# Performance work log

Measured on AMD Instinct MI355X. Metric: run time of the kernel, lower is better.

## Reference

```python
import jax, jax.numpy as jnp
import numpy as np

H, N, I, K = 1024, 16, 128, 2  # model dim, n_experts, expert inner dim (hardcoded in Expert), top-k
B, S = 4, 4096


def setup_inputs() -> dict:
    key = jax.random.key(0)
    ks = jax.random.split(key, 4)
    x = jax.random.normal(ks[0], (B, S, H), jnp.float32)
    Wr = jax.random.normal(ks[1], (N, H), jnp.float32) / np.sqrt(H)      # router Linear(h,n,bias=False) weight [n,h]
    Wg = jax.random.normal(ks[2], (N, I, H), jnp.float32) / np.sqrt(H)   # per-expert g: Linear(h,i) weight [i,h]
    bg = jnp.zeros((N, I), jnp.float32)
    Wu = jax.random.normal(ks[3], (N, H, I), jnp.float32) / np.sqrt(I)   # per-expert u: Linear(i,h) weight [h,i]
    bu = jnp.zeros((N, H), jnp.float32)
    return {"x": x, "Wr": Wr, "Wg": Wg, "bg": bg, "Wu": Wu, "bu": bu, "k": K}


def reference(x, Wr, Wg, bg, Wu, bu, k):
    b, s, h = x.shape
    n = Wr.shape[0]
    xf = x.reshape(-1, h)                      # [T, h]
    T = xf.shape[0]
    logits = xf @ Wr.T                          # [T, n]
    val, idx = jax.lax.top_k(logits, k)         # [T, k]
    w = jax.nn.softmax(val, axis=-1)            # softmax over selected top-k logits
    # scatter top-k weights into a dense [T, n] gate matrix (zero for unselected experts)
    gates = jnp.zeros((T, n), x.dtype).at[jnp.arange(T)[:, None], idx].set(w)
    # all-expert SwiGLU-free MLP: silu(x @ Wg^T + bg) @ Wu^T + bu, weighted combine by gates
    a = jax.nn.silu(jnp.einsum('th,nih->tni', xf, Wg) + bg)   # [T, n, i]
    out = jnp.einsum('tn,tni,nhi->th', gates, a, Wu) + gates @ bu
    return out.reshape(b, s, h)
```

## Files before the change

kernel.cpp:

```cpp
#include <hip/hip_runtime.h>
#include <hip/hip_fp16.h>

#define T_TOK 16384
#define HDIM  1024
#define NE    16
#define IDIM  128
#define BMq   64
#define NSLOT (T_TOK*2)
#define NSLOT_PAD (NSLOT + NE*BMq)
#define NBLK1 (NSLOT_PAD/BMq)

typedef _Float16 half8 __attribute__((ext_vector_type(8)));
typedef _Float16 half4 __attribute__((ext_vector_type(4)));
typedef float    f32x4 __attribute__((ext_vector_type(4)));

#define WS_TOKE 0
#define WS_TOKW 131072
#define WS_CNT  262144
#define WS_CUR  262208
#define WS_OFF  262272
#define WS_STOK 262400
#define WS_SW   397568
#define WS_ABUF 532736
#define WS_TSLOT 9183488ULL
#define WS_WG16  9314560ULL
#define WS_WU16  13508864ULL
#define WS_X16   17703168ULL
#define WS_OBUF  51257600ULL
#define WS_FULL_END 120463616ULL

template<bool WX>
__global__ __launch_bounds__(64) void router_k(const float* __restrict__ x,
                                               const float* __restrict__ Wr,
                                               int2* __restrict__ tok_e,
                                               float2* __restrict__ tok_w,
                                               _Float16* __restrict__ x16) {
    __shared__ __align__(16) _Float16 Ah[16*64], Al[16*64], Bh[16*64], Bl[16*64];
    int lane = threadIdx.x;
    int tile0 = blockIdx.x * 16;
    f32x4 accM = {0.f,0.f,0.f,0.f};
    f32x4 accC = {0.f,0.f,0.f,0.f};
    for (int kk = 0; kk < HDIM; kk += 64) {
        __syncthreads();
#pragma unroll
        for (int s = 0; s < 4; ++s) {
            int idx = lane + s*64;
            int r = idx >> 4, kq = idx & 15;
            float4 xv = *reinterpret_cast<const float4*>(x  + (size_t)(tile0 + r)*HDIM + kk + kq*4);
            float4 wv = *reinterpret_cast<const float4*>(Wr + (size_t)r*HDIM + kk + kq*4);
            half4 xh, xl, wh, wl;
            {
                float v0=xv.x,v1=xv.y,v2=xv.z,v3=xv.w;
                xh[0]=(_Float16)v0; xh[1]=(_Float16)v1; xh[2]=(_Float16)v2; xh[3]=(_Float16)v3;
                xl[0]=(_Float16)((v0-(float)xh[0])*2048.f); xl[1]=(_Float16)((v1-(float)xh[1])*2048.f);
                xl[2]=(_Float16)((v2-(float)xh[2])*2048.f); xl[3]=(_Float16)((v3-(float)xh[3])*2048.f);
                float w0=wv.x,w1=wv.y,w2=wv.z,w3=wv.w;
                wh[0]=(_Float16)w0; wh[1]=(_Float16)w1; wh[2]=(_Float16)w2; wh[3]=(_Float16)w3;
                wl[0]=(_Float16)((w0-(float)wh[0])*2048.f); wl[1]=(_Float16)((w1-(float)wh[1])*2048.f);
                wl[2]=(_Float16)((w2-(float)wh[2])*2048.f); wl[3]=(_Float16)((w3-(float)wh[3])*2048.f);
            }
            int sw = (kq*4) ^ ((r & 7) << 3);
            *reinterpret_cast<half4*>(&Ah[r*64 + sw]) = xh;
            *reinterpret_cast<half4*>(&Al[r*64 + sw]) = xl;
            *reinterpret_cast<half4*>(&Bh[r*64 + sw]) = wh;
            *reinterpret_cast<half4*>(&Bl[r*64 + sw]) = wl;
            if (WX)
                *reinterpret_cast<half4*>(x16 + (size_t)(tile0 + r)*HDIM + kk + kq*4) = xh;
        }
        __syncthreads();
        int rr = lane & 15;
        int swr = (rr & 7) << 3;
#pragma unroll
        for (int ks = 0; ks < 64; ks += 32) {
            int c = ks + ((lane >> 4) << 3);
            half8 axh = *reinterpret_cast<const half8*>(&Ah[rr*64 + (c ^ swr)]);
            half8 axl = *reinterpret_cast<const half8*>(&Al[rr*64 + (c ^ swr)]);
            half8 bwh = *reinterpret_cast<const half8*>(&Bh[rr*64 + (c ^ swr)]);
            half8 bwl = *reinterpret_cast<const half8*>(&Bl[rr*64 + (c ^ swr)]);
            accM = __builtin_amdgcn_mfma_f32_16x16x32_f16(axh, bwh, accM, 0, 0, 0);
            accC = __builtin_amdgcn_mfma_f32_16x16x32_f16(axh, bwl, accC, 0, 0, 0);
            accC = __builtin_amdgcn_mfma_f32_16x16x32_f16(axl, bwh, accC, 0, 0, 0);
        }
    }
    int c = lane & 15, g = lane >> 4;
#pragma unroll
    for (int j = 0; j < 4; ++j) {
        float v1 = accM[j] + accC[j] * (1.f/2048.f);
        int   i1 = c;
        float v2 = -1e30f; int i2 = 16;
#pragma unroll
        for (int m = 1; m < 16; m <<= 1) {
            float ov1 = __shfl_xor(v1, m); int oi1 = __shfl_xor(i1, m);
            float ov2 = __shfl_xor(v2, m); int oi2 = __shfl_xor(i2, m);
            float nv1, nv2; int ni1, ni2;
            bool aFirst = (v1 > ov1) || (v1 == ov1 && i1 < oi1);
            if (aFirst) {
                nv1 = v1; ni1 = i1;
                if ((v2 > ov1) || (v2 == ov1 && i2 < oi1)) { nv2 = v2; ni2 = i2; }
                else                                        { nv2 = ov1; ni2 = oi1; }
            } else {
                nv1 = ov1; ni1 = oi1;
                if ((ov2 > v1) || (ov2 == v1 && oi2 < i1)) { nv2 = ov2; ni2 = oi2; }
                else                                        { nv2 = v1; ni2 = i1; }
            }
            v1 = nv1; i1 = ni1; v2 = nv2; i2 = ni2;
        }
        if (c == 0) {
            int t = tile0 + g*4 + j;
            float e2 = __expf(v2 - v1);
            float inv = 1.f / (1.f + e2);
            tok_e[t] = make_int2(i1, i2);
            tok_w[t] = make_float2(inv, e2 * inv);
        }
    }
}

__global__ __launch_bounds__(256) void cvtw_k(const float* __restrict__ Wg,
                                              const float* __restrict__ Wu,
                                              _Float16* __restrict__ Wg16,
                                              _Float16* __restrict__ Wu16) {
    int i = blockIdx.x * 256 + threadIdx.x;
    float4 g = reinterpret_cast<const float4*>(Wg)[i];
    float4 u = reinterpret_cast<const float4*>(Wu)[i];
    half4 gh = {(_Float16)g.x,(_Float16)g.y,(_Float16)g.z,(_Float16)g.w};
    half4 uh = {(_Float16)u.x,(_Float16)u.y,(_Float16)u.z,(_Float16)u.w};
    reinterpret_cast<half4*>(Wg16)[i] = gh;
    reinterpret_cast<half4*>(Wu16)[i] = uh;
}

__global__ __launch_bounds__(256) void count_k(const int2* __restrict__ tok_e,
                                               int* __restrict__ counts) {
    int e = blockIdx.x;
    int c = 0;
    for (int t = threadIdx.x; t < T_TOK; t += 256) {
        int2 te = tok_e[t];
        c += (te.x == e) + (te.y == e);
    }
    __shared__ int red[256];
    red[threadIdx.x] = c; __syncthreads();
    for (int s = 128; s > 0; s >>= 1) {
        if (threadIdx.x < s) red[threadIdx.x] += red[threadIdx.x + s];
        __syncthreads();
    }
    if (threadIdx.x == 0) counts[e] = red[0];
}

__global__ void scan_k(const int* __restrict__ counts, int* __restrict__ offs) {
    if (threadIdx.x == 0) {
        int acc = 0;
        for (int e = 0; e < NE; ++e) {
            offs[e] = acc;
            acc += ((counts[e] + BMq - 1) / BMq) * BMq;
        }
        offs[NE] = acc;
    }
}

template<bool FULL>
__global__ __launch_bounds__(256) void scatter_k(const int2* __restrict__ tok_e,
                                                 const float2* __restrict__ tok_w,
                                                 const int* __restrict__ offs,
                                                 int* __restrict__ cursors,
                                                 int* __restrict__ slot_tok,
                                                 float* __restrict__ slot_w,
                                                 int2* __restrict__ tok_slots) {
    __shared__ int lcnt[NE];
    __shared__ int lbase[NE];
    if (threadIdx.x < NE) lcnt[threadIdx.x] = 0;
    __syncthreads();
    int t = blockIdx.x * 256 + threadIdx.x;
    int2 te = tok_e[t]; float2 tw = tok_w[t];
    int p0 = atomicAdd(&lcnt[te.x], 1);
    int p1 = atomicAdd(&lcnt[te.y], 1);
    __syncthreads();
    if (threadIdx.x < NE)
        lbase[threadIdx.x] = atomicAdd(&cursors[threadIdx.x], lcnt[threadIdx.x]);
    __syncthreads();
    int s0 = offs[te.x] + lbase[te.x] + p0;
    int s1 = offs[te.y] + lbase[te.y] + p1;
    slot_tok[s0] = t; slot_w[s0] = tw.x;
    slot_tok[s1] = t; slot_w[s1] = tw.y;
    if (FULL) tok_slots[t] = make_int2(s0, s1);
}

template<bool FULL>
__global__ __launch_bounds__(256) void gemm1_k(const float* __restrict__ x,
                                               const _Float16* __restrict__ x16,
                                               const float* __restrict__ Wg,
                                               const _Float16* __restrict__ Wg16,
                                               const float* __restrict__ bg,
                                               const int* __restrict__ offs,
                                               const int* __restrict__ slot_tok,
                                               _Float16* __restrict__ abuf) {
    __shared__ __align__(16) _Float16 As[64 * 64];
    __shared__ __align__(16) _Float16 Bs[128 * 64];
    __shared__ int tokLds[64];
    int row0 = blockIdx.x * BMq;
    if (row0 >= offs[NE]) return;
    int e = 0;
#pragma unroll
    for (int q = 1; q < NE; ++q) if (offs[q] <= row0) e = q;
    int tid = threadIdx.x;
    if (tid < 64) tokLds[tid] = slot_tok[row0 + tid];
    __syncthreads();
    int wv = tid >> 6, lane = tid & 63;
    f32x4 acc[4][2] = {};
    for (int kk = 0; kk < HDIM; kk += 64) {
        if (FULL) {
#pragma unroll
            for (int j = 0; j < 2; ++j) {
                int idx = tid + j * 256;
                int r = idx >> 3, hq = idx & 7;
                int tok = tokLds[r];
                half8 v = {0,0,0,0,0,0,0,0};
                if (tok >= 0) v = *reinterpret_cast<const half8*>(x16 + (size_t)tok * HDIM + kk + hq * 8);
                *reinterpret_cast<half8*>(&As[r * 64 + ((hq * 8) ^ ((r & 7) << 3))]) = v;
            }
#pragma unroll
            for (int j = 0; j < 4; ++j) {
                int idx = tid + j * 256;
                int r = idx >> 3, hq = idx & 7;
                half8 v = *reinterpret_cast<const half8*>(Wg16 + (size_t)e * IDIM * HDIM + (size_t)r * HDIM + kk + hq * 8);
                *reinterpret_cast<half8*>(&Bs[r * 64 + ((hq * 8) ^ ((r & 7) << 3))]) = v;
            }
        } else {
#pragma unroll
            for (int j = 0; j < 4; ++j) {
                int idx = tid + j * 256;
                int r = idx >> 4, kq = idx & 15;
                int tok = tokLds[r];
                float4 v = make_float4(0.f, 0.f, 0.f, 0.f);
                if (tok >= 0) v = *reinterpret_cast<const float4*>(x + (size_t)tok * HDIM + kk + kq * 4);
                half4 hv = {(_Float16)v.x, (_Float16)v.y, (_Float16)v.z, (_Float16)v.w};
                *reinterpret_cast<half4*>(&As[r * 64 + ((kq * 4) ^ ((r & 7) << 3))]) = hv;
            }
#pragma unroll 4
            for (int j = 0; j < 8; ++j) {
                int idx = tid + j * 256;
                int r = idx >> 4, kq = idx & 15;
                float4 v = *reinterpret_cast<const float4*>(Wg + (size_t)e * IDIM * HDIM + (size_t)r * HDIM + kk + kq * 4);
                half4 hv = {(_Float16)v.x, (_Float16)v.y, (_Float16)v.z, (_Float16)v.w};
                *reinterpret_cast<half4*>(&Bs[r * 64 + ((kq * 4) ^ ((r & 7) << 3))]) = hv;
            }
        }
        __syncthreads();
#pragma unroll
        for (int ks = 0; ks < 64; ks += 32) {
            int c = ks + ((lane >> 4) << 3);
            half8 af[4], bf[2];
#pragma unroll
            for (int rt = 0; rt < 4; ++rt) {
                int r = rt * 16 + (lane & 15);
                af[rt] = *reinterpret_cast<const half8*>(&As[r * 64 + (c ^ ((r & 7) << 3))]);
            }
#pragma unroll
            for (int ct = 0; ct < 2; ++ct) {
                int r = wv * 32 + ct * 16 + (lane & 15);
                bf[ct] = *reinterpret_cast<const half8*>(&Bs[r * 64 + (c ^ ((r & 7) << 3))]);
            }
#pragma unroll
            for (int rt = 0; rt < 4; ++rt)
#pragma unroll
                for (int ct = 0; ct < 2; ++ct)
                    acc[rt][ct] = __builtin_amdgcn_mfma_f32_16x16x32_f16(af[rt], bf[ct], acc[rt][ct], 0, 0, 0);
        }
        __syncthreads();
    }
#pragma unroll
    for (int rt = 0; rt < 4; ++rt)
#pragma unroll
        for (int ct = 0; ct < 2; ++ct) {
            int i = wv * 32 + ct * 16 + (lane & 15);
            float bgv = bg[e * IDIM + i];
#pragma unroll
            for (int j = 0; j < 4; ++j) {
                int m = rt * 16 + ((lane >> 4) << 2) + j;
                if (tokLds[m] >= 0) {
                    float v = acc[rt][ct][j] + bgv;
                    float sv = v / (1.f + __expf(-v));
                    abuf[(size_t)(row0 + m) * IDIM + i] = (_Float16)sv;
                }
            }
        }
}

template<bool FULL>
__global__ __launch_bounds__(256) void gemm2_k(const _Float16* __restrict__ abuf,
                                               const float* __restrict__ Wu,
                                               const _Float16* __restrict__ Wu16,
                                               const float* __restrict__ bu,
                                               const int* __restrict__ offs,
                                               const int* __restrict__ slot_tok,
                                               const float* __restrict__ slot_w,
                                               float* __restrict__ out,
                                               _Float16* __restrict__ Obuf) {
    __shared__ __align__(16) _Float16 As[64 * 128];
    __shared__ __align__(16) _Float16 Bs[128 * 128];
    __shared__ int   tokLds[64];
    __shared__ float wLds[64];
    int row0 = blockIdx.x * BMq;
    if (row0 >= offs[NE]) return;
    int h0 = blockIdx.y * 128;
    int e = 0;
#pragma unroll
    for (int q = 1; q < NE; ++q) if (offs[q] <= row0) e = q;
    int tid = threadIdx.x;
    if (tid < 64) { tokLds[tid] = slot_tok[row0 + tid]; wLds[tid] = slot_w[row0 + tid]; }
#pragma unroll
    for (int j = 0; j < 4; ++j) {
        int idx = tid + j * 256;
        int r = idx >> 4, hq = idx & 15;
        half8 v = *reinterpret_cast<const half8*>(abuf + (size_t)(row0 + r) * IDIM + hq * 8);
        *reinterpret_cast<half8*>(&As[r * 128 + ((hq * 8) ^ ((r & 7) << 3))]) = v;
    }
    if (FULL) {
#pragma unroll
        for (int j = 0; j < 8; ++j) {
            int idx = tid + j * 256;
            int r = idx >> 4, fq = idx & 15;
            half8 v = *reinterpret_cast<const half8*>(Wu16 + (size_t)e * HDIM * IDIM + (size_t)(h0 + r) * IDIM + fq * 8);
            *reinterpret_cast<half8*>(&Bs[r * 128 + ((fq * 8) ^ ((r & 7) << 3))]) = v;
        }
    } else {
#pragma unroll 4
        for (int j = 0; j < 16; ++j) {
            int idx = tid + j * 256;
            int r = idx >> 5, fq = idx & 31;
            float4 v = *reinterpret_cast<const float4*>(Wu + (size_t)e * HDIM * IDIM + (size_t)(h0 + r) * IDIM + fq * 4);
            half4 hv = {(_Float16)v.x, (_Float16)v.y, (_Float16)v.z, (_Float16)v.w};
            *reinterpret_cast<half4*>(&Bs[r * 128 + ((fq * 4) ^ ((r & 7) << 3))]) = hv;
        }
    }
    __syncthreads();
    int wv = tid >> 6, lane = tid & 63;
    f32x4 acc[4][2] = {};
#pragma unroll
    for (int ks = 0; ks < 128; ks += 32) {
        int c = ks + ((lane >> 4) << 3);
        half8 af[4], bf[2];
#pragma unroll
        for (int rt = 0; rt < 4; ++rt) {
            int r = rt * 16 + (lane & 15);
            af[rt] = *reinterpret_cast<const half8*>(&As[r * 128 + (c ^ ((r & 7) << 3))]);
        }
#pragma unroll
        for (int ct = 0; ct < 2; ++ct) {
            int r = wv * 32 + ct * 16 + (lane & 15);
            bf[ct] = *reinterpret_cast<const half8*>(&Bs[r * 128 + (c ^ ((r & 7) << 3))]);
        }
#pragma unroll
        for (int rt = 0; rt < 4; ++rt)
#pragma unroll
            for (int ct = 0; ct < 2; ++ct)
                acc[rt][ct] = __builtin_amdgcn_mfma_f32_16x16x32_f16(af[rt], bf[ct], acc[rt][ct], 0, 0, 0);
    }
#pragma unroll
    for (int rt = 0; rt < 4; ++rt)
#pragma unroll
        for (int ct = 0; ct < 2; ++ct) {
            int h = h0 + wv * 32 + ct * 16 + (lane & 15);
#pragma unroll
            for (int j = 0; j < 4; ++j) {
                int m = rt * 16 + ((lane >> 4) << 2) + j;
                if (FULL) {
                    Obuf[(size_t)(row0 + m) * HDIM + h] = (_Float16)acc[rt][ct][j];
                } else {
                    int tok = tokLds[m];
                    if (tok >= 0)
                        atomicAdd(out + (size_t)tok * HDIM + h,
                                  (acc[rt][ct][j] + bu[e * HDIM + h]) * wLds[m]);
                }
            }
        }
}

__global__ __launch_bounds__(256) void combine_k(const _Float16* __restrict__ Obuf,
                                                 const float* __restrict__ bu,
                                                 const int2* __restrict__ tok_slots,
                                                 const int2* __restrict__ tok_e,
                                                 const float2* __restrict__ tok_w,
                                                 float* __restrict__ out) {
    int wv = threadIdx.x >> 6, lane = threadIdx.x & 63;
    int t = blockIdx.x * 4 + wv;
    int2   sl = tok_slots[t];
    int2   te = tok_e[t];
    float2 tw = tok_w[t];
    const _Float16* O1 = Obuf + (size_t)sl.x * HDIM;
    const _Float16* O2 = Obuf + (size_t)sl.y * HDIM;
    const float* b1 = bu + (size_t)te.x * HDIM;
    const float* b2 = bu + (size_t)te.y * HDIM;
    float* op = out + (size_t)t * HDIM;
#pragma unroll
    for (int q = 0; q < 4; ++q) {
        int h = q * 256 + lane * 4;
        half4  a1 = *reinterpret_cast<const half4*>(O1 + h);
        half4  a2 = *reinterpret_cast<const half4*>(O2 + h);
        float4 v1 = *reinterpret_cast<const float4*>(b1 + h);
        float4 v2 = *reinterpret_cast<const float4*>(b2 + h);
        float4 o;
        o.x = tw.x * ((float)a1[0] + v1.x) + tw.y * ((float)a2[0] + v2.x);
        o.y = tw.x * ((float)a1[1] + v1.y) + tw.y * ((float)a2[1] + v2.y);
        o.z = tw.x * ((float)a1[2] + v1.z) + tw.y * ((float)a2[2] + v2.z);
        o.w = tw.x * ((float)a1[3] + v1.w) + tw.y * ((float)a2[3] + v2.w);
        *reinterpret_cast<float4*>(op + h) = o;
    }
}

extern "C" void kernel_launch(void* const* d_in, const int* in_sizes, int n_in,
                              void* d_out, int out_size, void* d_ws, size_t ws_size,
                              hipStream_t stream) {
    const float* x  = (const float*)d_in[0];
    const float* Wr = (const float*)d_in[1];
    const float* Wg = (const float*)d_in[2];
    const float* bg = (const float*)d_in[3];
    const float* Wu = (const float*)d_in[4];
    const float* bu = (const float*)d_in[5];
    float* out = (float*)d_out;
    char* ws = (char*)d_ws;

    int2*      tok_e    = (int2*)(ws + WS_TOKE);
    float2*    tok_w    = (float2*)(ws + WS_TOKW);
    int*       counts   = (int*)(ws + WS_CNT);
    int*       cursors  = (int*)(ws + WS_CUR);
    int*       offs     = (int*)(ws + WS_OFF);
    int*       slot_tok = (int*)(ws + WS_STOK);
    float*     slot_w   = (float*)(ws + WS_SW);
    _Float16*  abuf     = (_Float16*)(ws + WS_ABUF);
    int2*      tok_slots= (int2*)(ws + WS_TSLOT);
    _Float16*  Wg16     = (_Float16*)(ws + WS_WG16);
    _Float16*  Wu16     = (_Float16*)(ws + WS_WU16);
    _Float16*  x16      = (_Float16*)(ws + WS_X16);
    _Float16*  Obuf     = (_Float16*)(ws + WS_OBUF);

    const bool full = (ws_size >= WS_FULL_END);

    hipMemsetAsync(ws + WS_CNT, 0, 256, stream);
    hipMemsetAsync(slot_tok, 0xFF, NSLOT_PAD * sizeof(int), stream);

    if (full) {
        cvtw_k   <<<2048, 256, 0, stream>>>(Wg, Wu, Wg16, Wu16);
        router_k<true><<<T_TOK/16, 64, 0, stream>>>(x, Wr, tok_e, tok_w, x16);
        count_k  <<<NE, 256, 0, stream>>>(tok_e, counts);
        scan_k   <<<1, 64, 0, stream>>>(counts, offs);
        scatter_k<true><<<T_TOK/256, 256, 0, stream>>>(tok_e, tok_w, offs, cursors, slot_tok, slot_w, tok_slots);
        gemm1_k<true><<<NBLK1, 256, 0, stream>>>(x, x16, Wg, Wg16, bg, offs, slot_tok, abuf);
        dim3 g2(NBLK1, 8);
        gemm2_k<true><<<g2, 256, 0, stream>>>(abuf, Wu, Wu16, bu, offs, slot_tok, slot_w, out, Obuf);
        combine_k<<<T_TOK/4, 256, 0, stream>>>(Obuf, bu, tok_slots, tok_e, tok_w, out);
    } else {
        hipMemsetAsync(d_out, 0, (size_t)T_TOK * HDIM * sizeof(float), stream);
        router_k<false><<<T_TOK/16, 64, 0, stream>>>(x, Wr, tok_e, tok_w, nullptr);
        count_k  <<<NE, 256, 0, stream>>>(tok_e, counts);
        scan_k   <<<1, 64, 0, stream>>>(counts, offs);
        scatter_k<false><<<T_TOK/256, 256, 0, stream>>>(tok_e, tok_w, offs, cursors, slot_tok, slot_w, nullptr);
        gemm1_k<false><<<NBLK1, 256, 0, stream>>>(x, nullptr, Wg, nullptr, bg, offs, slot_tok, abuf);
        dim3 g2(NBLK1, 8);
        gemm2_k<false><<<g2, 256, 0, stream>>>(abuf, Wu, nullptr, bu, offs, slot_tok, slot_w, out, nullptr);
    }
}
```

Measured before the change: 285.3 us.

## Replace split-fp16 MFMA router with fp32 warp-per-token dot products

The router drops the hi/lo fp16 split MFMA GEMM with LDS staging and instead computes all 16 expert logits per token in fp32. Each wavefront handles one token at a time, with per-lane partial dot products and a butterfly shuffle reduction, then a serial top-2 in lane 0. This removes the LDS round trips, barriers and triple MFMA work, trading them for 16 full-wave shuffle reductions per token and repeated Wr loads that should mostly hit cache. The launch grid changes to 2048 blocks of 256 threads, each block covering 8 tokens.

New measurement: 274.8 us. -3.7%, faster.

```diff
diff --git a/kernel.cpp b/kernel.cpp
--- a/kernel.cpp
+++ b/kernel.cpp
@@ -30,83 +30,47 @@
 #define WS_FULL_END 120463616ULL
 
 template<bool WX>
-__global__ __launch_bounds__(64) void router_k(const float* __restrict__ x,
-                                               const float* __restrict__ Wr,
-                                               int2* __restrict__ tok_e,
-                                               float2* __restrict__ tok_w,
-                                               _Float16* __restrict__ x16) {
-    __shared__ __align__(16) _Float16 Ah[16*64], Al[16*64], Bh[16*64], Bl[16*64];
-    int lane = threadIdx.x;
-    int tile0 = blockIdx.x * 16;
-    f32x4 accM = {0.f,0.f,0.f,0.f};
-    f32x4 accC = {0.f,0.f,0.f,0.f};
-    for (int kk = 0; kk < HDIM; kk += 64) {
-        __syncthreads();
-#pragma unroll
-        for (int s = 0; s < 4; ++s) {
-            int idx = lane + s*64;
-            int r = idx >> 4, kq = idx & 15;
-            float4 xv = *reinterpret_cast<const float4*>(x  + (size_t)(tile0 + r)*HDIM + kk + kq*4);
-            float4 wv = *reinterpret_cast<const float4*>(Wr + (size_t)r*HDIM + kk + kq*4);
-            half4 xh, xl, wh, wl;
-            {
-                float v0=xv.x,v1=xv.y,v2=xv.z,v3=xv.w;
-                xh[0]=(_Float16)v0; xh[1]=(_Float16)v1; xh[2]=(_Float16)v2; xh[3]=(_Float16)v3;
-                xl[0]=(_Float16)((v0-(float)xh[0])*2048.f); xl[1]=(_Float16)((v1-(float)xh[1])*2048.f);
-                xl[2]=(_Float16)((v2-(float)xh[2])*2048.f); xl[3]=(_Float16)((v3-(float)xh[3])*2048.f);
-                float w0=wv.x,w1=wv.y,w2=wv.z,w3=wv.w;
-                wh[0]=(_Float16)w0; wh[1]=(_Float16)w1; wh[2]=(_Float16)w2; wh[3]=(_Float16)w3;
-                wl[0]=(_Float16)((w0-(float)wh[0])*2048.f); wl[1]=(_Float16)((w1-(float)wh[1])*2048.f);
-                wl[2]=(_Float16)((w2-(float)wh[2])*2048.f); wl[3]=(_Float16)((w3-(float)wh[3])*2048.f);
-            }
-            int sw = (kq*4) ^ ((r & 7) << 3);
-            *reinterpret_cast<half4*>(&Ah[r*64 + sw]) = xh;
-            *reinterpret_cast<half4*>(&Al[r*64 + sw]) = xl;
-            *reinterpret_cast<half4*>(&Bh[r*64 + sw]) = wh;
-            *reinterpret_cast<half4*>(&Bl[r*64 + sw]) = wl;
-            if (WX)
-                *reinterpret_cast<half4*>(x16 + (size_t)(tile0 + r)*HDIM + kk + kq*4) = xh;
-        }
-        __syncthreads();
-        int rr = lane & 15;
-        int swr = (rr & 7) << 3;
-#pragma unroll
-        for (int ks = 0; ks < 64; ks += 32) {
-            int c = ks + ((lane >> 4) << 3);
-            half8 axh = *reinterpret_cast<const half8*>(&Ah[rr*64 + (c ^ swr)]);
-            half8 axl = *reinterpret_cast<const half8*>(&Al[rr*64 + (c ^ swr)]);
-            half8 bwh = *reinterpret_cast<const half8*>(&Bh[rr*64 + (c ^ swr)]);
-            half8 bwl = *reinterpret_cast<const half8*>(&Bl[rr*64 + (c ^ swr)]);
-            accM = __builtin_amdgcn_mfma_f32_16x16x32_f16(axh, bwh, accM, 0, 0, 0);
-            accC = __builtin_amdgcn_mfma_f32_16x16x32_f16(axh, bwl, accC, 0, 0, 0);
-            accC = __builtin_amdgcn_mfma_f32_16x16x32_f16(axl, bwh, accC, 0, 0, 0);
-        }
-    }
-    int c = lane & 15, g = lane >> 4;
-#pragma unroll
-    for (int j = 0; j < 4; ++j) {
-        float v1 = accM[j] + accC[j] * (1.f/2048.f);
-        int   i1 = c;
-        float v2 = -1e30f; int i2 = 16;
-#pragma unroll
-        for (int m = 1; m < 16; m <<= 1) {
-            float ov1 = __shfl_xor(v1, m); int oi1 = __shfl_xor(i1, m);
-            float ov2 = __shfl_xor(v2, m); int oi2 = __shfl_xor(i2, m);
-            float nv1, nv2; int ni1, ni2;
-            bool aFirst = (v1 > ov1) || (v1 == ov1 && i1 < oi1);
-            if (aFirst) {
-                nv1 = v1; ni1 = i1;
-                if ((v2 > ov1) || (v2 == ov1 && i2 < oi1)) { nv2 = v2; ni2 = i2; }
-                else                                        { nv2 = ov1; ni2 = oi1; }
-            } else {
-                nv1 = ov1; ni1 = oi1;
-                if ((ov2 > v1) || (ov2 == v1 && oi2 < i1)) { nv2 = ov2; ni2 = oi2; }
-                else                                        { nv2 = v1; ni2 = i1; }
-            }
-            v1 = nv1; i1 = ni1; v2 = nv2; i2 = ni2;
-        }
-        if (c == 0) {
-            int t = tile0 + g*4 + j;
+__global__ __launch_bounds__(256) void router_k(const float* __restrict__ x,
+                                                const float* __restrict__ Wr,
+                                                int2* __restrict__ tok_e,
+                                                float2* __restrict__ tok_w,
+                                                _Float16* __restrict__ x16) {
+    int wv = threadIdx.x >> 6, lane = threadIdx.x & 63;
+#pragma unroll
+    for (int i = 0; i < 2; ++i) {
+        int t = blockIdx.x * 4 + wv + i * 8192;
+        float acc[NE];
+#pragma unroll
+        for (int e = 0; e < NE; ++e) acc[e] = 0.f;
+        const float4* xp = reinterpret_cast<const float4*>(x + (size_t)t * HDIM);
+#pragma unroll
+        for (int p = 0; p < 4; ++p) {
+            int off = p * 64 + lane;
+            float4 xv = xp[off];
+            if (WX) {
+                half4 hv = {(_Float16)xv.x,(_Float16)xv.y,(_Float16)xv.z,(_Float16)xv.w};
+                *reinterpret_cast<half4*>(x16 + (size_t)t * HDIM + off * 4) = hv;
+            }
+#pragma unroll
+            for (int e = 0; e < NE; ++e) {
+                float4 wv4 = *reinterpret_cast<const float4*>(Wr + (size_t)e * HDIM + off * 4);
+                acc[e] += xv.x*wv4.x + xv.y*wv4.y + xv.z*wv4.z + xv.w*wv4.w;
+            }
+        }
+#pragma unroll
+        for (int e = 0; e < NE; ++e) {
+#pragma unroll
+            for (int m = 1; m < 64; m <<= 1)
+                acc[e] += __shfl_xor(acc[e], m);
+        }
+        if (lane == 0) {
+            float v1 = -1e30f, v2 = -1e30f; int i1 = 0, i2 = 0;
+#pragma unroll
+            for (int q = 0; q < NE; ++q) {
+                float lv = acc[q];
+                if (lv > v1)      { v2 = v1; i2 = i1; v1 = lv; i1 = q; }
+                else if (lv > v2) { v2 = lv; i2 = q; }
+            }
             float e2 = __expf(v2 - v1);
             float inv = 1.f / (1.f + e2);
             tok_e[t] = make_int2(i1, i2);
@@ -439,7 +403,7 @@
 
     if (full) {
         cvtw_k   <<<2048, 256, 0, stream>>>(Wg, Wu, Wg16, Wu16);
-        router_k<true><<<T_TOK/16, 64, 0, stream>>>(x, Wr, tok_e, tok_w, x16);
+        router_k<true><<<T_TOK/8, 256, 0, stream>>>(x, Wr, tok_e, tok_w, x16);
         count_k  <<<NE, 256, 0, stream>>>(tok_e, counts);
         scan_k   <<<1, 64, 0, stream>>>(counts, offs);
         scatter_k<true><<<T_TOK/256, 256, 0, stream>>>(tok_e, tok_w, offs, cursors, slot_tok, slot_w, tok_slots);
@@ -449,7 +413,7 @@
         combine_k<<<T_TOK/4, 256, 0, stream>>>(Obuf, bu, tok_slots, tok_e, tok_w, out);
     } else {
         hipMemsetAsync(d_out, 0, (size_t)T_TOK * HDIM * sizeof(float), stream);
-        router_k<false><<<T_TOK/16, 64, 0, stream>>>(x, Wr, tok_e, tok_w, nullptr);
+        router_k<false><<<T_TOK/8, 256, 0, stream>>>(x, Wr, tok_e, tok_w, nullptr);
         count_k  <<<NE, 256, 0, stream>>>(tok_e, counts);
         scan_k   <<<1, 64, 0, stream>>>(counts, offs);
         scatter_k<false><<<T_TOK/256, 256, 0, stream>>>(tok_e, tok_w, offs, cursors, slot_tok, slot_w, nullptr);
```
